# Kernel optimization log

Hardware: AMD Instinct MI355X
Metric: run time of the kernel (lower is better)

Reference implementation:

```python
import jax, jax.numpy as jnp
import numpy as np

VOCAB, EMB, WIN = 32000, 300, 5
H1, H2, NY, NZ = 300, 300, 128, 128
B, S = 32, 512


def setup_inputs() -> dict:
    key = jax.random.key(0)
    ks = jax.random.split(key, 16)
    sc = 0.05
    inp = {
        "x": jax.random.randint(ks[0], (B, S, WIN), 0, VOCAB),
        "emb": jax.random.normal(ks[1], (VOCAB, EMB), jnp.float32) * sc,
        "W_ih1": jax.random.normal(ks[2], (H1, EMB * WIN), jnp.float32) * sc,
        "W_hh1": jax.random.normal(ks[3], (H1, H1), jnp.float32) * sc,
        "b_ih1": jax.random.normal(ks[4], (H1,), jnp.float32) * sc,
        "b_hh1": jax.random.normal(ks[5], (H1,), jnp.float32) * sc,
        "W_ih2": jax.random.normal(ks[6], (H2, H1), jnp.float32) * sc,
        "W_hh2": jax.random.normal(ks[7], (H2, H2), jnp.float32) * sc,
        "b_ih2": jax.random.normal(ks[8], (H2,), jnp.float32) * sc,
        "b_hh2": jax.random.normal(ks[9], (H2,), jnp.float32) * sc,
        "fc1_w": jax.random.normal(ks[10], (NY, H1), jnp.float32) * sc,
        "fc1_b": jax.random.normal(ks[11], (NY,), jnp.float32) * sc,
        "fc2_w": jax.random.normal(ks[12], (NZ, H2), jnp.float32) * sc,
        "fc2_b": jax.random.normal(ks[13], (NZ,), jnp.float32) * sc,
    }
    return inp


def reference(x, emb, W_ih1, W_hh1, b_ih1, b_hh1, W_ih2, W_hh2, b_ih2, b_hh2,
              fc1_w, fc1_b, fc2_w, fc2_b):
    b, s, w = x.shape
    xe = emb[jnp.transpose(x, (1, 0, 2))].reshape(s, b, w * emb.shape[1])
    xe = jax.nn.relu(xe)

    h1_0 = jnp.zeros((b, W_hh1.shape[0]), xe.dtype)
    h2_0 = jnp.zeros((b, W_hh2.shape[0]), xe.dtype)

    def step(carry, xt):
        h1, h2 = carry
        h1 = jnp.tanh(xt @ W_ih1.T + b_ih1 + h1 @ W_hh1.T + b_hh1)
        h2 = jnp.tanh(h1 @ W_ih2.T + b_ih2 + h2 @ W_hh2.T + b_hh2)
        return (h1, h2), (h1, h2)

    _, (out1, out2) = jax.lax.scan(step, (h1_0, h2_0), xe)  # [S,B,H]

    out1 = jnp.transpose(out1, (1, 0, 2)).reshape(b * s, -1)
    out2 = jnp.transpose(out2, (1, 0, 2)).reshape(b * s, -1)
    out1 = out1 @ fc1_w.T + fc1_b
    out2 = out2 @ fc2_w.T + fc2_b
    return (out1, out2)
```

## Files before the change

### kernel.cpp

```cpp
#include <hip/hip_runtime.h>
#include <hip/hip_fp16.h>

#define S_LEN 512
#define BATCH 32
#define CHUNK 16

typedef _Float16 hv2  __attribute__((ext_vector_type(2)));
typedef _Float16 half8 __attribute__((ext_vector_type(8)));
typedef float    f32x4 __attribute__((ext_vector_type(4)));

__device__ __forceinline__ float dot2f(hv2 a, hv2 b, float c) {
#if __has_builtin(__builtin_amdgcn_fdot2)
    return __builtin_amdgcn_fdot2(a, b, c, false);
#else
    return c + (float)a.x * (float)b.x + (float)a.y * (float)b.y;
#endif
}

__device__ __forceinline__ float fast_tanh(float x) {
    float e = __expf(2.f * x);
    return 1.f - 2.f / (e + 1.f);
}

__device__ __forceinline__ void lds_barrier() {
    __asm__ volatile("s_waitcnt lgkmcnt(0)\n\ts_barrier" ::: "memory");
}
__device__ __forceinline__ void vm_drain() {
    __asm__ volatile("s_waitcnt vmcnt(0)" ::: "memory");
}

#define E8   1280000
#define W18  64000
#define W28  12800
#define FF8  5120
#define PREP_TOTAL8 (E8 + W18 + W28 + FF8 + FF8)

__global__ __launch_bounds__(256) void k_prep(
    const float* __restrict__ emb,  const float* __restrict__ Wih1,
    const float* __restrict__ Wih2, const float* __restrict__ fc1w,
    const float* __restrict__ fc2w,
    _Float16* __restrict__ embf, _Float16* __restrict__ Wf1,
    _Float16* __restrict__ Wf2,  _Float16* __restrict__ F1,
    _Float16* __restrict__ F2,   unsigned int* __restrict__ flags)
{
    int gid = blockIdx.x * 256 + threadIdx.x;
    if (gid < 64) flags[gid] = 0u;
    if (gid >= PREP_TOTAL8) return;

    half8 v;
    _Float16* dst;

    if (gid < E8) {
        int row = gid / 40, c8 = (gid - row * 40) * 8;
        #pragma unroll
        for (int j = 0; j < 8; ++j) {
            int c = c8 + j;
            float f = (c < 300) ? emb[(size_t)row * 300 + c] : 0.f;
            v[j] = (_Float16)(f > 0.f ? f : 0.f);
        }
        dst = embf + (size_t)gid * 8;
    } else if (gid < E8 + W18) {
        int i = gid - E8;
        int row = i / 200, c8 = (i - row * 200) * 8;
        #pragma unroll
        for (int j = 0; j < 8; ++j) {
            int c = c8 + j, w = c / 320, cc = c - w * 320;
            float f = (row < 300 && cc < 300) ? Wih1[(size_t)row * 1500 + w * 300 + cc] : 0.f;
            v[j] = (_Float16)f;
        }
        dst = Wf1 + (size_t)i * 8;
    } else if (gid < E8 + W18 + W28) {
        int i = gid - E8 - W18;
        int row = i / 40, c8 = (i - row * 40) * 8;
        #pragma unroll
        for (int j = 0; j < 8; ++j) {
            int c = c8 + j;
            float f = (row < 300 && c < 300) ? Wih2[(size_t)row * 300 + c] : 0.f;
            v[j] = (_Float16)f;
        }
        dst = Wf2 + (size_t)i * 8;
    } else if (gid < E8 + W18 + W28 + FF8) {
        int i = gid - E8 - W18 - W28;
        int row = i / 40, c8 = (i - row * 40) * 8;
        #pragma unroll
        for (int j = 0; j < 8; ++j) {
            int c = c8 + j;
            v[j] = (_Float16)((c < 300) ? fc1w[(size_t)row * 300 + c] : 0.f);
        }
        dst = F1 + (size_t)i * 8;
    } else {
        int i = gid - E8 - W18 - W28 - FF8;
        int row = i / 40, c8 = (i - row * 40) * 8;
        #pragma unroll
        for (int j = 0; j < 8; ++j) {
            int c = c8 + j;
            v[j] = (_Float16)((c < 300) ? fc2w[(size_t)row * 300 + c] : 0.f);
        }
        dst = F2 + (size_t)i * 8;
    }
    *(half8*)dst = v;
}

__global__ __launch_bounds__(256) void k_gemm1_mfma(
    const int* __restrict__ x, const _Float16* __restrict__ embf,
    const _Float16* __restrict__ Wf1, const float* __restrict__ b1,
    const float* __restrict__ b2, float* __restrict__ U)
{
    const int wid  = threadIdx.x >> 6;
    const int lane = threadIdx.x & 63;
    const int m    = lane & 15;
    const int q    = lane >> 4;
    const int r0   = blockIdx.x * 128 + wid * 32;
    const int n0   = blockIdx.y * 160;

    f32x4 acc[2][10];
    #pragma unroll
    for (int i = 0; i < 2; ++i)
        #pragma unroll
        for (int j = 0; j < 10; ++j)
            acc[i][j] = (f32x4){0.f, 0.f, 0.f, 0.f};

    const int rA = r0 + m, rB = r0 + 16 + m;
    const int xbA = ((rA & 31) * S_LEN + (rA >> 5)) * 5;
    const int xbB = ((rB & 31) * S_LEN + (rB >> 5)) * 5;

    for (int w = 0; w < 5; ++w) {
        const int idxA = x[xbA + w];
        const int idxB = x[xbB + w];
        const _Float16* ea = embf + (size_t)idxA * 320;
        const _Float16* eb = embf + (size_t)idxB * 320;
        const _Float16* wb = Wf1 + (size_t)w * 320;
        #pragma unroll
        for (int c = 0; c < 10; ++c) {
            const int k = c * 32 + q * 8;
            half8 a0 = *(const half8*)(ea + k);
            half8 a1 = *(const half8*)(eb + k);
            #pragma unroll
            for (int nt = 0; nt < 10; ++nt) {
                half8 bf = *(const half8*)(wb + (size_t)(n0 + nt * 16 + m) * 1600 + k);
                acc[0][nt] = __builtin_amdgcn_mfma_f32_16x16x32_f16(a0, bf, acc[0][nt], 0, 0, 0);
                acc[1][nt] = __builtin_amdgcn_mfma_f32_16x16x32_f16(a1, bf, acc[1][nt], 0, 0, 0);
            }
        }
    }

    #pragma unroll
    for (int nt = 0; nt < 10; ++nt) {
        const int n = n0 + nt * 16 + m;
        if (n >= 300) continue;
        const float bias = b1[n] + b2[n];
        #pragma unroll
        for (int mt = 0; mt < 2; ++mt) {
            const int rbase = r0 + mt * 16 + q * 4;
            #pragma unroll
            for (int reg = 0; reg < 4; ++reg)
                U[(size_t)(rbase + reg) * 300 + n] = acc[mt][nt][reg] + bias;
        }
    }
}

__global__ __launch_bounds__(256) void k_fc_mfma(
    const _Float16* __restrict__ H1, const _Float16* __restrict__ H2,
    const _Float16* __restrict__ F1, const _Float16* __restrict__ F2,
    const float* __restrict__ fb1, const float* __restrict__ fb2,
    float* __restrict__ out1, float* __restrict__ out2)
{
    const int layer = blockIdx.y;
    const _Float16* H = layer ? H2 : H1;
    const _Float16* F = layer ? F2 : F1;
    const float* bias = layer ? fb2 : fb1;
    float* out        = layer ? out2 : out1;

    const int wid  = threadIdx.x >> 6;
    const int lane = threadIdx.x & 63;
    const int m    = lane & 15;
    const int q    = lane >> 4;
    const int r0   = blockIdx.x * 128 + wid * 32;

    f32x4 acc[2][8];
    #pragma unroll
    for (int i = 0; i < 2; ++i)
        #pragma unroll
        for (int j = 0; j < 8; ++j)
            acc[i][j] = (f32x4){0.f, 0.f, 0.f, 0.f};

    const _Float16* ha = H + (size_t)(r0 + m) * 320;
    const _Float16* hb = H + (size_t)(r0 + 16 + m) * 320;

    #pragma unroll
    for (int c = 0; c < 10; ++c) {
        const int k = c * 32 + q * 8;
        half8 a0 = *(const half8*)(ha + k);
        half8 a1 = *(const half8*)(hb + k);
        #pragma unroll
        for (int nt = 0; nt < 8; ++nt) {
            half8 bf = *(const half8*)(F + (size_t)(nt * 16 + m) * 320 + k);
            acc[0][nt] = __builtin_amdgcn_mfma_f32_16x16x32_f16(a0, bf, acc[0][nt], 0, 0, 0);
            acc[1][nt] = __builtin_amdgcn_mfma_f32_16x16x32_f16(a1, bf, acc[1][nt], 0, 0, 0);
        }
    }

    #pragma unroll
    for (int nt = 0; nt < 8; ++nt) {
        const int n = nt * 16 + m;
        const float bv = bias[n];
        #pragma unroll
        for (int mt = 0; mt < 2; ++mt) {
            #pragma unroll
            for (int reg = 0; reg < 4; ++reg) {
                const int r = r0 + mt * 16 + q * 4 + reg;
                const int oidx = ((r & 31) * S_LEN + (r >> 5)) * 128 + n;
                out[oidx] = acc[mt][nt][reg] + bv;
            }
        }
    }
}

#define LDS_BYTES 60416

__device__ __forceinline__ void load_u_regs(float* up, const float* __restrict__ U1,
                                            int b, int t0) {
    #pragma unroll
    for (int j = 0; j < 10; ++j) {
        int e = threadIdx.x + 512 * j;
        int row = e / 300, col = e - row * 300;
        up[j] = (e < 4800) ? U1[((size_t)((t0 + row) * BATCH + b)) * 300 + col] : 0.f;
    }
}

__global__ __launch_bounds__(512) void k_rec_fused(
    const float* __restrict__ U1, const float* __restrict__ Whh1,
    const _Float16* __restrict__ Wf2, const float* __restrict__ Whh2,
    const float* __restrict__ bih2, const float* __restrict__ bhh2,
    _Float16* __restrict__ H1f, _Float16* __restrict__ H2f,
    unsigned int* __restrict__ flags)
{
    extern __shared__ char smem[];
    float    (*partials)[8][320] = (float(*)[8][320])smem;
    _Float16 (*hc)[320]  = (_Float16(*)[320])(smem + 20480);
    float    (*uc)[304]  = (float(*)[304])(smem + 30720);
    char*     h1sb       = smem + 50176;

    const int tid  = threadIdx.x;
    const int wv   = tid >> 6;
    const int lane = tid & 63;
    const int r    = wv * 40 + lane;
    const bool prod = blockIdx.x < 32;
    const int b    = prod ? (int)blockIdx.x : (int)blockIdx.x - 32;

    for (int i = tid; i < CHUNK * 320; i += 512)
        ((_Float16*)hc)[i] = (_Float16)0.f;

    const float* Whh = prod ? Whh1 : Whh2;
    hv2 wreg[5][20];
    #pragma unroll
    for (int i = 0; i < 5; ++i) {
        const int row = lane + 64 * i;
        const float* wrow = Whh + (size_t)row * 300 + 40 * wv;
        #pragma unroll
        for (int j = 0; j < 20; ++j) {
            const int c0 = 40 * wv + 2 * j;
            hv2 p;
            p.x = (row < 300 && c0     < 300) ? (_Float16)wrow[2 * j]     : (_Float16)0.f;
            p.y = (row < 300 && c0 + 1 < 300) ? (_Float16)wrow[2 * j + 1] : (_Float16)0.f;
            wreg[i][j] = p;
        }
    }

    const float biasc = (!prod && lane < 40 && r < 300) ? (bih2[r] + bhh2[r]) : 0.f;

    unsigned hpk = 0u;

    auto do_step = [&](int s) {
        const int par = s & 1;
        float a0 = 0.f, a1 = 0.f, a2 = 0.f, a3 = 0.f, a4 = 0.f;
        #pragma unroll
        for (int j = 0; j < 20; ++j) {
            const unsigned hj = __builtin_amdgcn_readlane(hpk, j);
            const hv2 hvv = __builtin_bit_cast(hv2, hj);
            a0 = dot2f(wreg[0][j], hvv, a0);
            a1 = dot2f(wreg[1][j], hvv, a1);
            a2 = dot2f(wreg[2][j], hvv, a2);
            a3 = dot2f(wreg[3][j], hvv, a3);
            a4 = dot2f(wreg[4][j], hvv, a4);
        }
        partials[par][wv][lane      ] = a0;
        partials[par][wv][lane +  64] = a1;
        partials[par][wv][lane + 128] = a2;
        partials[par][wv][lane + 192] = a3;
        partials[par][wv][lane + 256] = a4;
        const bool act = (lane < 40) && (r < 300);
        float uval = act ? (uc[s][r] + biasc) : 0.f;
        lds_barrier();
        float v = 0.f;
        if (act) {
            float s01 = partials[par][0][r] + partials[par][1][r];
            float s23 = partials[par][2][r] + partials[par][3][r];
            float s45 = partials[par][4][r] + partials[par][5][r];
            float s67 = partials[par][6][r] + partials[par][7][r];
            v = fast_tanh(uval + ((s01 + s23) + (s45 + s67)));
            hc[s][r] = (_Float16)v;
        }
        const float pa = __shfl(v, 2 * lane);
        const float pb = __shfl(v, 2 * lane + 1);
        hv2 hp2; hp2.x = (_Float16)pa; hp2.y = (_Float16)pb;
        hpk = __builtin_bit_cast(unsigned, hp2);
    };

    if (prod) {
        float upref[10];
        load_u_regs(upref, U1, b, 0);

        for (int c = 0; c < 32; ++c) {
            const int t0 = c * CHUNK;
            if (c > 0) {
                const int tb = t0 - CHUNK;
                for (int i = tid; i < CHUNK * 40; i += 512) {
                    int row = i / 40, c8 = i - row * 40;
                    half8 vv = *(const half8*)&hc[row][c8 * 8];
                    *(half8*)&H1f[((size_t)((tb + row) * BATCH + b)) * 320 + c8 * 8] = vv;
                }
            }
            #pragma unroll
            for (int j = 0; j < 10; ++j) {
                int e = tid + 512 * j;
                if (e < 4800) {
                    int row = e / 300, col = e - row * 300;
                    uc[row][col] = upref[j];
                }
            }
            if (c > 0) {
                vm_drain();
                if (tid == 0)
                    __hip_atomic_store(&flags[b], (unsigned)t0,
                                       __ATOMIC_RELEASE, __HIP_MEMORY_SCOPE_AGENT);
            }
            if (c + 1 < 32)
                load_u_regs(upref, U1, b, t0 + CHUNK);
            lds_barrier();

            for (int s = 0; s < CHUNK; ++s) do_step(s);
            lds_barrier();
        }
        {
            const int tb = S_LEN - CHUNK;
            for (int i = tid; i < CHUNK * 40; i += 512) {
                int row = i / 40, c8 = i - row * 40;
                half8 vv = *(const half8*)&hc[row][c8 * 8];
                *(half8*)&H1f[((size_t)((tb + row) * BATCH + b)) * 320 + c8 * 8] = vv;
            }
            vm_drain();
            if (tid == 0)
                __hip_atomic_store(&flags[b], (unsigned)S_LEN,
                                   __ATOMIC_RELEASE, __HIP_MEMORY_SCOPE_AGENT);
        }
    } else {
        for (int c = 0; c < 32; ++c) {
            const int t0 = c * CHUNK;
            if (c > 0) {
                const int tb = t0 - CHUNK;
                for (int i = tid; i < CHUNK * 40; i += 512) {
                    int row = i / 40, c8 = i - row * 40;
                    half8 vv = *(const half8*)&hc[row][c8 * 8];
                    *(half8*)&H2f[((size_t)((tb + row) * BATCH + b)) * 320 + c8 * 8] = vv;
                }
            }
            if (tid == 0) {
                while (__hip_atomic_load(&flags[b], __ATOMIC_ACQUIRE,
                                         __HIP_MEMORY_SCOPE_AGENT) < (unsigned)(t0 + CHUNK))
                    __builtin_amdgcn_s_sleep(2);
            }
            __syncthreads();

            for (int i = tid; i < CHUNK * 40; i += 512) {
                int row = i / 40, c8 = i - row * 40;
                half8 vv = *(const half8*)&H1f[((size_t)((t0 + row) * BATCH + b)) * 320 + c8 * 8];
                *(half8*)(h1sb + row * 640 + ((c8 * 16) ^ ((row & 7) << 4))) = vv;
            }
            lds_barrier();

            {
                const int lm = lane & 15, lq = lane >> 4;
                for (int nt = wv; nt < 19; nt += 8) {
                    f32x4 acc = (f32x4){0.f, 0.f, 0.f, 0.f};
                    const int n = nt * 16 + lm;
                    const _Float16* wrow2 = Wf2 + (size_t)n * 320;
                    #pragma unroll
                    for (int k0 = 0; k0 < 320; k0 += 32) {
                        half8 av = *(const half8*)(h1sb + lm * 640 +
                                    (((k0 + lq * 8) * 2) ^ ((lm & 7) << 4)));
                        half8 bf = *(const half8*)&wrow2[k0 + lq * 8];
                        acc = __builtin_amdgcn_mfma_f32_16x16x32_f16(av, bf, acc, 0, 0, 0);
                    }
                    #pragma unroll
                    for (int reg = 0; reg < 4; ++reg)
                        uc[lq * 4 + reg][n] = acc[reg];
                }
            }
            lds_barrier();

            for (int s = 0; s < CHUNK; ++s) do_step(s);
            lds_barrier();
        }
        {
            const int tb = S_LEN - CHUNK;
            for (int i = tid; i < CHUNK * 40; i += 512) {
                int row = i / 40, c8 = i - row * 40;
                half8 vv = *(const half8*)&hc[row][c8 * 8];
                *(half8*)&H2f[((size_t)((tb + row) * BATCH + b)) * 320 + c8 * 8] = vv;
            }
        }
    }
}

extern "C" void kernel_launch(void* const* d_in, const int* in_sizes, int n_in,
                              void* d_out, int out_size, void* d_ws, size_t ws_size,
                              hipStream_t stream) {
    const int*   x     = (const int*)d_in[0];
    const float* emb   = (const float*)d_in[1];
    const float* Wih1  = (const float*)d_in[2];
    const float* Whh1  = (const float*)d_in[3];
    const float* bih1  = (const float*)d_in[4];
    const float* bhh1  = (const float*)d_in[5];
    const float* Wih2  = (const float*)d_in[6];
    const float* Whh2  = (const float*)d_in[7];
    const float* bih2  = (const float*)d_in[8];
    const float* bhh2  = (const float*)d_in[9];
    const float* fc1w  = (const float*)d_in[10];
    const float* fc1b  = (const float*)d_in[11];
    const float* fc2w  = (const float*)d_in[12];
    const float* fc2b  = (const float*)d_in[13];

    float* out1 = (float*)d_out;
    float* out2 = out1 + (size_t)16384 * 128;

    char* w = (char*)d_ws;
    float*        U1    = (float*)w;
    _Float16*     H1    = (_Float16*)(w + 19660800);
    _Float16*     Wf1   = (_Float16*)(w + 30146560);
    _Float16*     Wf2   = (_Float16*)(w + 31170560);
    _Float16*     F1    = (_Float16*)(w + 31375360);
    _Float16*     F2    = (_Float16*)(w + 31457280);
    unsigned int* flags = (unsigned int*)(w + 31539200);
    _Float16*     EMBF  = (_Float16*)(w + 31539456);
    _Float16*     H2    = EMBF;

    const int prep_blocks = (PREP_TOTAL8 + 255) / 256;
    k_prep<<<prep_blocks, 256, 0, stream>>>(emb, Wih1, Wih2, fc1w, fc2w,
                                            EMBF, Wf1, Wf2, F1, F2, flags);

    dim3 g(128, 2);
    k_gemm1_mfma<<<g, 256, 0, stream>>>(x, EMBF, Wf1, bih1, bhh1, U1);
    k_rec_fused<<<64, 512, LDS_BYTES, stream>>>(U1, Whh1, Wf2, Whh2, bih2, bhh2,
                                                H1, H2, flags);
    k_fc_mfma<<<g, 256, 0, stream>>>(H1, H2, F1, F2, fc1b, fc2b, out1, out2);
}
```

Before: 902.0 us.

## Fuse both RNN layers into one block per batch with skewed chunk pipeline

Replaces the producer/consumer pair of blocks linked by global flags with a single 512-thread block per batch element. Four waves run layer 1 and four run layer 2 one chunk behind, sharing hidden states through an LDS ring buffer. This removes the global-memory flag handshake and the H1 reload for layer 2. The U1 intermediate is stored as fp16 to halve its traffic. Each wave now holds twice as many recurrent weights in registers (80 columns instead of 40), which raises register pressure. Only 32 blocks run instead of 64, and every step now has two barriers covering both layers.

New measurement: 1.426 ms. 58.1% more time.

```diff
diff --git a/kernel.cpp b/kernel.cpp
--- a/kernel.cpp
+++ b/kernel.cpp
@@ -25,9 +25,6 @@
 __device__ __forceinline__ void lds_barrier() {
     __asm__ volatile("s_waitcnt lgkmcnt(0)\n\ts_barrier" ::: "memory");
 }
-__device__ __forceinline__ void vm_drain() {
-    __asm__ volatile("s_waitcnt vmcnt(0)" ::: "memory");
-}
 
 #define E8   1280000
 #define W18  64000
@@ -41,10 +38,9 @@
     const float* __restrict__ fc2w,
     _Float16* __restrict__ embf, _Float16* __restrict__ Wf1,
     _Float16* __restrict__ Wf2,  _Float16* __restrict__ F1,
-    _Float16* __restrict__ F2,   unsigned int* __restrict__ flags)
+    _Float16* __restrict__ F2)
 {
     int gid = blockIdx.x * 256 + threadIdx.x;
-    if (gid < 64) flags[gid] = 0u;
     if (gid >= PREP_TOTAL8) return;
 
     half8 v;
@@ -104,7 +100,7 @@
 __global__ __launch_bounds__(256) void k_gemm1_mfma(
     const int* __restrict__ x, const _Float16* __restrict__ embf,
     const _Float16* __restrict__ Wf1, const float* __restrict__ b1,
-    const float* __restrict__ b2, float* __restrict__ U)
+    const float* __restrict__ b2, _Float16* __restrict__ U)
 {
     const int wid  = threadIdx.x >> 6;
     const int lane = threadIdx.x & 63;
@@ -154,7 +150,7 @@
             const int rbase = r0 + mt * 16 + q * 4;
             #pragma unroll
             for (int reg = 0; reg < 4; ++reg)
-                U[(size_t)(rbase + reg) * 300 + n] = acc[mt][nt][reg] + bias;
+                U[(size_t)(rbase + reg) * 300 + n] = (_Float16)(acc[mt][nt][reg] + bias);
         }
     }
 }
@@ -216,199 +212,193 @@
     }
 }
 
-#define LDS_BYTES 60416
-
-__device__ __forceinline__ void load_u_regs(float* up, const float* __restrict__ U1,
-                                            int b, int t0) {
-    #pragma unroll
-    for (int j = 0; j < 10; ++j) {
-        int e = threadIdx.x + 512 * j;
-        int row = e / 300, col = e - row * 300;
-        up[j] = (e < 4800) ? U1[((size_t)((t0 + row) * BATCH + b)) * 300 + col] : 0.f;
+#define LDS_BYTES 80256
+
+__device__ __forceinline__ void load_u_pairs(hv2* up, const _Float16* __restrict__ U1h,
+                                             int b, int t0) {
+    #pragma unroll
+    for (int k = 0; k < 5; ++k) {
+        int p = threadIdx.x + 512 * k;
+        if (p < 2400) {
+            int row = p / 150, col2 = (p - row * 150) * 2;
+            up[k] = *(const hv2*)&U1h[((size_t)((t0 + row) * BATCH + b)) * 300 + col2];
+        } else {
+            up[k] = (hv2){(_Float16)0.f, (_Float16)0.f};
+        }
     }
 }
 
 __global__ __launch_bounds__(512) void k_rec_fused(
-    const float* __restrict__ U1, const float* __restrict__ Whh1,
+    const _Float16* __restrict__ U1h, const float* __restrict__ Whh1,
     const _Float16* __restrict__ Wf2, const float* __restrict__ Whh2,
     const float* __restrict__ bih2, const float* __restrict__ bhh2,
-    _Float16* __restrict__ H1f, _Float16* __restrict__ H2f,
-    unsigned int* __restrict__ flags)
+    _Float16* __restrict__ H1f, _Float16* __restrict__ H2f)
 {
     extern __shared__ char smem[];
-    float    (*partials)[8][320] = (float(*)[8][320])smem;
-    _Float16 (*hc)[320]  = (_Float16(*)[320])(smem + 20480);
-    float    (*uc)[304]  = (float(*)[304])(smem + 30720);
-    char*     h1sb       = smem + 50176;
+    float* p1   = (float*)smem;
+    float* p2   = (float*)(smem + 5120);
+    char*  hc1b = smem + 10240;
+    char*  hc2b = smem + 30720;
+    _Float16* uc1h = (_Float16*)(smem + 51200);
+    float (*uc2)[304] = (float(*)[304])(smem + 60800);
 
     const int tid  = threadIdx.x;
-    const int wv   = tid >> 6;
+    const int wid  = tid >> 6;
     const int lane = tid & 63;
-    const int r    = wv * 40 + lane;
-    const bool prod = blockIdx.x < 32;
-    const int b    = prod ? (int)blockIdx.x : (int)blockIdx.x - 32;
-
-    for (int i = tid; i < CHUNK * 320; i += 512)
-        ((_Float16*)hc)[i] = (_Float16)0.f;
-
-    const float* Whh = prod ? Whh1 : Whh2;
-    hv2 wreg[5][20];
-    #pragma unroll
-    for (int i = 0; i < 5; ++i) {
-        const int row = lane + 64 * i;
-        const float* wrow = Whh + (size_t)row * 300 + 40 * wv;
-        #pragma unroll
-        for (int j = 0; j < 20; ++j) {
-            const int c0 = 40 * wv + 2 * j;
-            hv2 p;
-            p.x = (row < 300 && c0     < 300) ? (_Float16)wrow[2 * j]     : (_Float16)0.f;
-            p.y = (row < 300 && c0 + 1 < 300) ? (_Float16)wrow[2 * j + 1] : (_Float16)0.f;
-            wreg[i][j] = p;
-        }
-    }
-
-    const float biasc = (!prod && lane < 40 && r < 300) ? (bih2[r] + bhh2[r]) : 0.f;
-
-    unsigned hpk = 0u;
-
-    auto do_step = [&](int s) {
-        const int par = s & 1;
-        float a0 = 0.f, a1 = 0.f, a2 = 0.f, a3 = 0.f, a4 = 0.f;
-        #pragma unroll
-        for (int j = 0; j < 20; ++j) {
-            const unsigned hj = __builtin_amdgcn_readlane(hpk, j);
-            const hv2 hvv = __builtin_bit_cast(hv2, hj);
-            a0 = dot2f(wreg[0][j], hvv, a0);
-            a1 = dot2f(wreg[1][j], hvv, a1);
-            a2 = dot2f(wreg[2][j], hvv, a2);
-            a3 = dot2f(wreg[3][j], hvv, a3);
-            a4 = dot2f(wreg[4][j], hvv, a4);
-        }
-        partials[par][wv][lane      ] = a0;
-        partials[par][wv][lane +  64] = a1;
-        partials[par][wv][lane + 128] = a2;
-        partials[par][wv][lane + 192] = a3;
-        partials[par][wv][lane + 256] = a4;
-        const bool act = (lane < 40) && (r < 300);
-        float uval = act ? (uc[s][r] + biasc) : 0.f;
+    const int b    = blockIdx.x;
+    const bool isL1 = (wid < 4);
+    const int  ws   = wid & 3;
+    float* pt = isL1 ? p1 : p2;
+
+    for (int i = tid; i < 5120; i += 512)
+        ((half8*)hc1b)[i] = (half8){0,0,0,0,0,0,0,0};
+
+    hv2 wreg[5][40];
+    {
+        const float* W = isL1 ? Whh1 : Whh2;
+        #pragma unroll
+        for (int i = 0; i < 5; ++i) {
+            const int row = lane + 64 * i;
+            const bool rok = row < 300;
+            const float* wr = W + (size_t)row * 300 + 80 * ws;
+            #pragma unroll
+            for (int j = 0; j < 40; ++j) {
+                const int c0 = 80 * ws + 2 * j;
+                hv2 p;
+                p.x = (rok && c0     < 300) ? (_Float16)wr[2 * j]     : (_Float16)0.f;
+                p.y = (rok && c0 + 1 < 300) ? (_Float16)wr[2 * j + 1] : (_Float16)0.f;
+                wreg[i][j] = p;
+            }
+        }
+    }
+
+    const float b2r = (tid < 300) ? (bih2[tid] + bhh2[tid]) : 0.f;
+
+    hv2 upref[5];
+    load_u_pairs(upref, U1h, b, 0);
+
+    for (int c = 0; c <= 32; ++c) {
+        if (c >= 1) {
+            const int tb = (c - 1) * CHUNK;
+            for (int i = tid; i < CHUNK * 40; i += 512) {
+                int rrow = i / 40, c8 = i - rrow * 40;
+                int ring = (tb + rrow) & 31;
+                half8 vv = *(const half8*)(hc1b + ring * 640 +
+                                           ((c8 * 16) ^ ((ring & 7) << 4)));
+                *(half8*)&H1f[((size_t)((tb + rrow) * BATCH + b)) * 320 + c8 * 8] = vv;
+            }
+        }
+        if (c >= 2) {
+            const int tb = (c - 2) * CHUNK;
+            for (int i = tid; i < CHUNK * 40; i += 512) {
+                int rrow = i / 40, c8 = i - rrow * 40;
+                int ring = (tb + rrow) & 31;
+                half8 vv = *(const half8*)(hc2b + ring * 640 +
+                                           ((c8 * 16) ^ ((ring & 7) << 4)));
+                *(half8*)&H2f[((size_t)((tb + rrow) * BATCH + b)) * 320 + c8 * 8] = vv;
+            }
+        }
+
+        if (c < 32) {
+            #pragma unroll
+            for (int k = 0; k < 5; ++k) {
+                int p = tid + 512 * k;
+                if (p < 2400) {
+                    int prow = p / 150, pc2 = (p - prow * 150) * 2;
+                    *(hv2*)&uc1h[(size_t)prow * 300 + pc2] = upref[k];
+                }
+            }
+            if (c + 1 < 32)
+                load_u_pairs(upref, U1h, b, (c + 1) * CHUNK);
+        }
+
+        if (c >= 1) {
+            const int R0 = ((c - 1) * CHUNK) & 31;
+            const int lm = lane & 15, lq = lane >> 4;
+            for (int nt = wid; nt < 19; nt += 8) {
+                f32x4 acc = (f32x4){0.f, 0.f, 0.f, 0.f};
+                const int n = nt * 16 + lm;
+                const _Float16* wrow = Wf2 + (size_t)n * 320;
+                #pragma unroll
+                for (int k0 = 0; k0 < 10; ++k0) {
+                    const int row = R0 + lm;
+                    half8 av = *(const half8*)(hc1b + row * 640 +
+                                 ((k0 * 64 + lq * 16) ^ ((row & 7) << 4)));
+                    half8 bf = *(const half8*)&wrow[k0 * 32 + lq * 8];
+                    acc = __builtin_amdgcn_mfma_f32_16x16x32_f16(av, bf, acc, 0, 0, 0);
+                }
+                #pragma unroll
+                for (int reg = 0; reg < 4; ++reg)
+                    uc2[lq * 4 + reg][n] = acc[reg];
+            }
+        }
         lds_barrier();
-        float v = 0.f;
-        if (act) {
-            float s01 = partials[par][0][r] + partials[par][1][r];
-            float s23 = partials[par][2][r] + partials[par][3][r];
-            float s45 = partials[par][4][r] + partials[par][5][r];
-            float s67 = partials[par][6][r] + partials[par][7][r];
-            v = fast_tanh(uval + ((s01 + s23) + (s45 + s67)));
-            hc[s][r] = (_Float16)v;
-        }
-        const float pa = __shfl(v, 2 * lane);
-        const float pb = __shfl(v, 2 * lane + 1);
-        hv2 hp2; hp2.x = (_Float16)pa; hp2.y = (_Float16)pb;
-        hpk = __builtin_bit_cast(unsigned, hp2);
-    };
-
-    if (prod) {
-        float upref[10];
-        load_u_regs(upref, U1, b, 0);
-
-        for (int c = 0; c < 32; ++c) {
-            const int t0 = c * CHUNK;
-            if (c > 0) {
-                const int tb = t0 - CHUNK;
-                for (int i = tid; i < CHUNK * 40; i += 512) {
-                    int row = i / 40, c8 = i - row * 40;
-                    half8 vv = *(const half8*)&hc[row][c8 * 8];
-                    *(half8*)&H1f[((size_t)((tb + row) * BATCH + b)) * 320 + c8 * 8] = vv;
+
+        #pragma unroll 1
+        for (int s = 0; s < CHUNK; ++s) {
+            float u1v = 0.f, u2v = 0.f;
+            if (tid < 300) {
+                if (c < 32) u1v = (float)uc1h[(size_t)s * 300 + tid];
+                if (c >= 1) u2v = uc2[s][tid] + b2r;
+            }
+            const bool aact = isL1 ? (c < 32) : (c >= 1);
+            if (aact) {
+                const int tm1 = (isL1 ? (c * CHUNK + s) : (c * CHUNK + s - CHUNK)) - 1;
+                const int rr = tm1 & 31;
+                const char* rowp = (isL1 ? hc1b : hc2b) + rr * 640;
+                const int sw = (rr & 7) << 4;
+                float a0 = 0.f, a1 = 0.f, a2 = 0.f, a3 = 0.f, a4 = 0.f;
+                #pragma unroll
+                for (int jj = 0; jj < 10; ++jj) {
+                    half8 q8 = *(const half8*)(rowp + ((ws * 160 + jj * 16) ^ sw));
+                    const hv2* qv = (const hv2*)&q8;
+                    #pragma unroll
+                    for (int j4 = 0; j4 < 4; ++j4) {
+                        const int j = jj * 4 + j4;
+                        a0 = dot2f(wreg[0][j], qv[j4], a0);
+                        a1 = dot2f(wreg[1][j], qv[j4], a1);
+                        a2 = dot2f(wreg[2][j], qv[j4], a2);
+                        a3 = dot2f(wreg[3][j], qv[j4], a3);
+                        a4 = dot2f(wreg[4][j], qv[j4], a4);
+                    }
                 }
-            }
-            #pragma unroll
-            for (int j = 0; j < 10; ++j) {
-                int e = tid + 512 * j;
-                if (e < 4800) {
-                    int row = e / 300, col = e - row * 300;
-                    uc[row][col] = upref[j];
+                pt[ws * 320 + lane      ] = a0;
+                pt[ws * 320 + lane +  64] = a1;
+                pt[ws * 320 + lane + 128] = a2;
+                pt[ws * 320 + lane + 192] = a3;
+                pt[ws * 320 + lane + 256] = a4;
+            }
+            lds_barrier();
+            if (tid < 300) {
+                if (c < 32) {
+                    float sm = (p1[tid] + p1[320 + tid]) +
+                               (p1[640 + tid] + p1[960 + tid]);
+                    float h = fast_tanh(u1v + sm);
+                    const int wr = (c * CHUNK + s) & 31;
+                    *(_Float16*)(hc1b + wr * 640 + ((tid * 2) ^ ((wr & 7) << 4))) =
+                        (_Float16)h;
                 }
-            }
-            if (c > 0) {
-                vm_drain();
-                if (tid == 0)
-                    __hip_atomic_store(&flags[b], (unsigned)t0,
-                                       __ATOMIC_RELEASE, __HIP_MEMORY_SCOPE_AGENT);
-            }
-            if (c + 1 < 32)
-                load_u_regs(upref, U1, b, t0 + CHUNK);
+                if (c >= 1) {
+                    float sm = (p2[tid] + p2[320 + tid]) +
+                               (p2[640 + tid] + p2[960 + tid]);
+                    float h = fast_tanh(u2v + sm);
+                    const int wr = (c * CHUNK + s - CHUNK) & 31;
+                    *(_Float16*)(hc2b + wr * 640 + ((tid * 2) ^ ((wr & 7) << 4))) =
+                        (_Float16)h;
+                }
+            }
             lds_barrier();
-
-            for (int s = 0; s < CHUNK; ++s) do_step(s);
-            lds_barrier();
-        }
-        {
-            const int tb = S_LEN - CHUNK;
-            for (int i = tid; i < CHUNK * 40; i += 512) {
-                int row = i / 40, c8 = i - row * 40;
-                half8 vv = *(const half8*)&hc[row][c8 * 8];
-                *(half8*)&H1f[((size_t)((tb + row) * BATCH + b)) * 320 + c8 * 8] = vv;
-            }
-            vm_drain();
-            if (tid == 0)
-                __hip_atomic_store(&flags[b], (unsigned)S_LEN,
-                                   __ATOMIC_RELEASE, __HIP_MEMORY_SCOPE_AGENT);
-        }
-    } else {
-        for (int c = 0; c < 32; ++c) {
-            const int t0 = c * CHUNK;
-            if (c > 0) {
-                const int tb = t0 - CHUNK;
-                for (int i = tid; i < CHUNK * 40; i += 512) {
-                    int row = i / 40, c8 = i - row * 40;
-                    half8 vv = *(const half8*)&hc[row][c8 * 8];
-                    *(half8*)&H2f[((size_t)((tb + row) * BATCH + b)) * 320 + c8 * 8] = vv;
-                }
-            }
-            if (tid == 0) {
-                while (__hip_atomic_load(&flags[b], __ATOMIC_ACQUIRE,
-                                         __HIP_MEMORY_SCOPE_AGENT) < (unsigned)(t0 + CHUNK))
-                    __builtin_amdgcn_s_sleep(2);
-            }
-            __syncthreads();
-
-            for (int i = tid; i < CHUNK * 40; i += 512) {
-                int row = i / 40, c8 = i - row * 40;
-                half8 vv = *(const half8*)&H1f[((size_t)((t0 + row) * BATCH + b)) * 320 + c8 * 8];
-                *(half8*)(h1sb + row * 640 + ((c8 * 16) ^ ((row & 7) << 4))) = vv;
-            }
-            lds_barrier();
-
-            {
-                const int lm = lane & 15, lq = lane >> 4;
-                for (int nt = wv; nt < 19; nt += 8) {
-                    f32x4 acc = (f32x4){0.f, 0.f, 0.f, 0.f};
-                    const int n = nt * 16 + lm;
-                    const _Float16* wrow2 = Wf2 + (size_t)n * 320;
-                    #pragma unroll
-                    for (int k0 = 0; k0 < 320; k0 += 32) {
-                        half8 av = *(const half8*)(h1sb + lm * 640 +
-                                    (((k0 + lq * 8) * 2) ^ ((lm & 7) << 4)));
-                        half8 bf = *(const half8*)&wrow2[k0 + lq * 8];
-                        acc = __builtin_amdgcn_mfma_f32_16x16x32_f16(av, bf, acc, 0, 0, 0);
-                    }
-                    #pragma unroll
-                    for (int reg = 0; reg < 4; ++reg)
-                        uc[lq * 4 + reg][n] = acc[reg];
-                }
-            }
-            lds_barrier();
-
-            for (int s = 0; s < CHUNK; ++s) do_step(s);
-            lds_barrier();
-        }
-        {
-            const int tb = S_LEN - CHUNK;
-            for (int i = tid; i < CHUNK * 40; i += 512) {
-                int row = i / 40, c8 = i - row * 40;
-                half8 vv = *(const half8*)&hc[row][c8 * 8];
-                *(half8*)&H2f[((size_t)((tb + row) * BATCH + b)) * 320 + c8 * 8] = vv;
-            }
+        }
+    }
+
+    {
+        const int tb = S_LEN - CHUNK;
+        for (int i = tid; i < CHUNK * 40; i += 512) {
+            int rrow = i / 40, c8 = i - rrow * 40;
+            int ring = (tb + rrow) & 31;
+            half8 vv = *(const half8*)(hc2b + ring * 640 +
+                                       ((c8 * 16) ^ ((ring & 7) << 4)));
+            *(half8*)&H2f[((size_t)((tb + rrow) * BATCH + b)) * 320 + c8 * 8] = vv;
         }
     }
 }
@@ -435,23 +425,22 @@
     float* out2 = out1 + (size_t)16384 * 128;
 
     char* w = (char*)d_ws;
-    float*        U1    = (float*)w;
+    _Float16*     U1    = (_Float16*)w;
     _Float16*     H1    = (_Float16*)(w + 19660800);
     _Float16*     Wf1   = (_Float16*)(w + 30146560);
     _Float16*     Wf2   = (_Float16*)(w + 31170560);
     _Float16*     F1    = (_Float16*)(w + 31375360);
     _Float16*     F2    = (_Float16*)(w + 31457280);
-    unsigned int* flags = (unsigned int*)(w + 31539200);
     _Float16*     EMBF  = (_Float16*)(w + 31539456);
     _Float16*     H2    = EMBF;
 
     const int prep_blocks = (PREP_TOTAL8 + 255) / 256;
     k_prep<<<prep_blocks, 256, 0, stream>>>(emb, Wih1, Wih2, fc1w, fc2w,
-                                            EMBF, Wf1, Wf2, F1, F2, flags);
+                                            EMBF, Wf1, Wf2, F1, F2);
 
     dim3 g(128, 2);
     k_gemm1_mfma<<<g, 256, 0, stream>>>(x, EMBF, Wf1, bih1, bhh1, U1);
-    k_rec_fused<<<64, 512, LDS_BYTES, stream>>>(U1, Whh1, Wf2, Whh2, bih2, bhh2,
-                                                H1, H2, flags);
+    k_rec_fused<<<32, 512, LDS_BYTES, stream>>>(U1, Whh1, Wf2, Whh2, bih2, bhh2,
+                                                H1, H2);
     k_fc_mfma<<<g, 256, 0, stream>>>(H1, H2, F1, F2, fc1b, fc2b, out1, out2);
 }
```

## Rewrite recurrence as batched MFMA over 16-batch tiles with separate Wih2 projection blocks

Applied to the files above, without the earlier changes.

Replaces the per-batch recurrence, which used dot2 products, readlane broadcasts and an 8-wave partial-sum reduction in LDS, with an MFMA recurrence. Each of four blocks handles 16 batch columns of one layer, keeping Whh in registers and passing h through double-buffered LDS. Four extra blocks compute the layer-2 input projection in chunks of 16 steps, synchronised with the recurrence blocks through global flags. U1 is now stored in fp16 with padded stride 304, which cuts memory traffic but uses only 8 blocks on the GPU and adds fp16 rounding of the pre-activations.

Result: slower. 1.116 ms (+23.7%).

```diff
diff --git a/kernel.cpp b/kernel.cpp
--- a/kernel.cpp
+++ b/kernel.cpp
@@ -3,19 +3,11 @@
 
 #define S_LEN 512
 #define BATCH 32
-#define CHUNK 16
 
 typedef _Float16 hv2  __attribute__((ext_vector_type(2)));
+typedef _Float16 hv4  __attribute__((ext_vector_type(4)));
 typedef _Float16 half8 __attribute__((ext_vector_type(8)));
 typedef float    f32x4 __attribute__((ext_vector_type(4)));
-
-__device__ __forceinline__ float dot2f(hv2 a, hv2 b, float c) {
-#if __has_builtin(__builtin_amdgcn_fdot2)
-    return __builtin_amdgcn_fdot2(a, b, c, false);
-#else
-    return c + (float)a.x * (float)b.x + (float)a.y * (float)b.y;
-#endif
-}
 
 __device__ __forceinline__ float fast_tanh(float x) {
     float e = __expf(2.f * x);
@@ -104,7 +96,7 @@
 __global__ __launch_bounds__(256) void k_gemm1_mfma(
     const int* __restrict__ x, const _Float16* __restrict__ embf,
     const _Float16* __restrict__ Wf1, const float* __restrict__ b1,
-    const float* __restrict__ b2, float* __restrict__ U)
+    const float* __restrict__ b2, _Float16* __restrict__ U)
 {
     const int wid  = threadIdx.x >> 6;
     const int lane = threadIdx.x & 63;
@@ -147,14 +139,14 @@
     #pragma unroll
     for (int nt = 0; nt < 10; ++nt) {
         const int n = n0 + nt * 16 + m;
-        if (n >= 300) continue;
-        const float bias = b1[n] + b2[n];
+        if (n >= 304) continue;
+        const float bias = (n < 300) ? (b1[n] + b2[n]) : 0.f;
         #pragma unroll
         for (int mt = 0; mt < 2; ++mt) {
             const int rbase = r0 + mt * 16 + q * 4;
             #pragma unroll
             for (int reg = 0; reg < 4; ++reg)
-                U[(size_t)(rbase + reg) * 300 + n] = acc[mt][nt][reg] + bias;
+                U[(size_t)(rbase + reg) * 304 + n] = (_Float16)(acc[mt][nt][reg] + bias);
         }
     }
 }
@@ -170,6 +162,7 @@
     const _Float16* F = layer ? F2 : F1;
     const float* bias = layer ? fb2 : fb1;
     float* out        = layer ? out2 : out1;
+    const int hs      = layer ? 304 : 320;
 
     const int wid  = threadIdx.x >> 6;
     const int lane = threadIdx.x & 63;
@@ -184,8 +177,8 @@
         for (int j = 0; j < 8; ++j)
             acc[i][j] = (f32x4){0.f, 0.f, 0.f, 0.f};
 
-    const _Float16* ha = H + (size_t)(r0 + m) * 320;
-    const _Float16* hb = H + (size_t)(r0 + 16 + m) * 320;
+    const _Float16* ha = H + (size_t)(r0 + m) * hs;
+    const _Float16* hb = H + (size_t)(r0 + 16 + m) * hs;
 
     #pragma unroll
     for (int c = 0; c < 10; ++c) {
@@ -216,199 +209,193 @@
     }
 }
 
-#define LDS_BYTES 60416
-
-__device__ __forceinline__ void load_u_regs(float* up, const float* __restrict__ U1,
-                                            int b, int t0) {
-    #pragma unroll
-    for (int j = 0; j < 10; ++j) {
-        int e = threadIdx.x + 512 * j;
-        int row = e / 300, col = e - row * 300;
-        up[j] = (e < 4800) ? U1[((size_t)((t0 + row) * BATCH + b)) * 300 + col] : 0.f;
-    }
-}
-
-__global__ __launch_bounds__(512) void k_rec_fused(
-    const float* __restrict__ U1, const float* __restrict__ Whh1,
-    const _Float16* __restrict__ Wf2, const float* __restrict__ Whh2,
+#define REC_LDS 20480
+
+__global__ __launch_bounds__(640) void k_rec(
+    const _Float16* __restrict__ U1h, _Float16* __restrict__ U2f,
+    const float* __restrict__ Whh1, const float* __restrict__ Whh2,
+    const _Float16* __restrict__ Wf2,
     const float* __restrict__ bih2, const float* __restrict__ bhh2,
     _Float16* __restrict__ H1f, _Float16* __restrict__ H2f,
     unsigned int* __restrict__ flags)
 {
     extern __shared__ char smem[];
-    float    (*partials)[8][320] = (float(*)[8][320])smem;
-    _Float16 (*hc)[320]  = (_Float16(*)[320])(smem + 20480);
-    float    (*uc)[304]  = (float(*)[304])(smem + 30720);
-    char*     h1sb       = smem + 50176;
-
-    const int tid  = threadIdx.x;
-    const int wv   = tid >> 6;
-    const int lane = tid & 63;
-    const int r    = wv * 40 + lane;
-    const bool prod = blockIdx.x < 32;
-    const int b    = prod ? (int)blockIdx.x : (int)blockIdx.x - 32;
-
-    for (int i = tid; i < CHUNK * 320; i += 512)
-        ((_Float16*)hc)[i] = (_Float16)0.f;
-
-    const float* Whh = prod ? Whh1 : Whh2;
-    hv2 wreg[5][20];
-    #pragma unroll
-    for (int i = 0; i < 5; ++i) {
-        const int row = lane + 64 * i;
-        const float* wrow = Whh + (size_t)row * 300 + 40 * wv;
-        #pragma unroll
-        for (int j = 0; j < 20; ++j) {
-            const int c0 = 40 * wv + 2 * j;
-            hv2 p;
-            p.x = (row < 300 && c0     < 300) ? (_Float16)wrow[2 * j]     : (_Float16)0.f;
-            p.y = (row < 300 && c0 + 1 < 300) ? (_Float16)wrow[2 * j + 1] : (_Float16)0.f;
-            wreg[i][j] = p;
-        }
-    }
-
-    const float biasc = (!prod && lane < 40 && r < 300) ? (bih2[r] + bhh2[r]) : 0.f;
-
-    unsigned hpk = 0u;
-
-    auto do_step = [&](int s) {
-        const int par = s & 1;
-        float a0 = 0.f, a1 = 0.f, a2 = 0.f, a3 = 0.f, a4 = 0.f;
-        #pragma unroll
-        for (int j = 0; j < 20; ++j) {
-            const unsigned hj = __builtin_amdgcn_readlane(hpk, j);
-            const hv2 hvv = __builtin_bit_cast(hv2, hj);
-            a0 = dot2f(wreg[0][j], hvv, a0);
-            a1 = dot2f(wreg[1][j], hvv, a1);
-            a2 = dot2f(wreg[2][j], hvv, a2);
-            a3 = dot2f(wreg[3][j], hvv, a3);
-            a4 = dot2f(wreg[4][j], hvv, a4);
-        }
-        partials[par][wv][lane      ] = a0;
-        partials[par][wv][lane +  64] = a1;
-        partials[par][wv][lane + 128] = a2;
-        partials[par][wv][lane + 192] = a3;
-        partials[par][wv][lane + 256] = a4;
-        const bool act = (lane < 40) && (r < 300);
-        float uval = act ? (uc[s][r] + biasc) : 0.f;
+    const int tid = threadIdx.x;
+    const int wv  = tid >> 6;
+    const int l   = tid & 63;
+    const int m   = l & 15;
+    const int q   = l >> 4;
+    const int bix = blockIdx.x;
+
+    if (bix < 4) {
+        const int layer = bix >> 1;
+        const int nb0   = (bix & 1) * 16;
+        const int batch = nb0 + m;
+        const float* W  = layer ? Whh2 : Whh1;
+        const _Float16* uP = layer ? U2f : U1h;
+        _Float16* hOut  = layer ? H2f : H1f;
+        const int hs    = layer ? 304 : 320;
+
+        half8 aw0[10], aw1[10];
+        {
+            const int rm0 = 32 * wv + m, rm1 = rm0 + 16;
+            #pragma unroll
+            for (int kt = 0; kt < 10; ++kt) {
+                #pragma unroll
+                for (int j = 0; j < 8; ++j) {
+                    const int k = kt * 32 + q * 8 + j;
+                    const bool kok = k < 300;
+                    aw0[kt][j] = (rm0 < 300 && kok) ? (_Float16)W[(size_t)rm0 * 300 + k]
+                                                    : (_Float16)0.f;
+                    aw1[kt][j] = (rm1 < 300 && kok) ? (_Float16)W[(size_t)rm1 * 300 + k]
+                                                    : (_Float16)0.f;
+                }
+            }
+        }
+        const int r0w = 32 * wv + q * 4;
+        const int sw  = (m & 7) << 4;
+        const bool uok1 = (32 * wv + 16) < 304;
+
+        int roff[10];
+        #pragma unroll
+        for (int kt = 0; kt < 10; ++kt)
+            roff[kt] = m * 640 + ((kt * 64 + q * 16) ^ sw);
+        const int woff0 = m * 640 + ((r0w * 2) ^ sw);
+        const int woff1 = m * 640 + (((r0w + 16) * 2) ^ sw);
+
+        half8 z8 = {};
+        ((half8*)smem)[tid] = z8;
         lds_barrier();
-        float v = 0.f;
-        if (act) {
-            float s01 = partials[par][0][r] + partials[par][1][r];
-            float s23 = partials[par][2][r] + partials[par][3][r];
-            float s45 = partials[par][4][r] + partials[par][5][r];
-            float s67 = partials[par][6][r] + partials[par][7][r];
-            v = fast_tanh(uval + ((s01 + s23) + (s45 + s67)));
-            hc[s][r] = (_Float16)v;
-        }
-        const float pa = __shfl(v, 2 * lane);
-        const float pb = __shfl(v, 2 * lane + 1);
-        hv2 hp2; hp2.x = (_Float16)pa; hp2.y = (_Float16)pb;
-        hpk = __builtin_bit_cast(unsigned, hp2);
-    };
-
-    if (prod) {
-        float upref[10];
-        load_u_regs(upref, U1, b, 0);
-
-        for (int c = 0; c < 32; ++c) {
-            const int t0 = c * CHUNK;
-            if (c > 0) {
-                const int tb = t0 - CHUNK;
-                for (int i = tid; i < CHUNK * 40; i += 512) {
-                    int row = i / 40, c8 = i - row * 40;
-                    half8 vv = *(const half8*)&hc[row][c8 * 8];
-                    *(half8*)&H1f[((size_t)((tb + row) * BATCH + b)) * 320 + c8 * 8] = vv;
+
+        hv4 u0 = {}, u1 = {};
+        if (!layer) {
+            u0 = *(const hv4*)&uP[(size_t)batch * 304 + r0w];
+            if (uok1) u1 = *(const hv4*)&uP[(size_t)batch * 304 + r0w + 16];
+        }
+
+        for (int t = 0; t < 512; ++t) {
+            char* rb = smem + (t & 1) * 10240;
+            char* wb = smem + ((t + 1) & 1) * 10240;
+            if (layer && (t & 15) == 0) {
+                if (tid == 0) {
+                    while (__hip_atomic_load(&flags[2 + (t >> 4)], __ATOMIC_ACQUIRE,
+                                             __HIP_MEMORY_SCOPE_AGENT) == 0)
+                        __builtin_amdgcn_s_sleep(8);
                 }
-            }
-            #pragma unroll
-            for (int j = 0; j < 10; ++j) {
-                int e = tid + 512 * j;
-                if (e < 4800) {
-                    int row = e / 300, col = e - row * 300;
-                    uc[row][col] = upref[j];
+                __syncthreads();
+                u0 = *(const hv4*)&uP[(size_t)(t * 32 + batch) * 304 + r0w];
+                if (uok1) u1 = *(const hv4*)&uP[(size_t)(t * 32 + batch) * 304 + r0w + 16];
+            }
+            f32x4 acc0, acc1;
+            #pragma unroll
+            for (int r = 0; r < 4; ++r) {
+                acc0[r] = (float)u0[r];
+                acc1[r] = (float)u1[r];
+            }
+            const int tn = t + 1;
+            if (tn < 512 && (!layer || (tn & 15) != 0)) {
+                u0 = *(const hv4*)&uP[(size_t)(tn * 32 + batch) * 304 + r0w];
+                if (uok1) u1 = *(const hv4*)&uP[(size_t)(tn * 32 + batch) * 304 + r0w + 16];
+            }
+            #pragma unroll
+            for (int kt = 0; kt < 10; ++kt) {
+                half8 bf = *(const half8*)(rb + roff[kt]);
+                acc0 = __builtin_amdgcn_mfma_f32_16x16x32_f16(aw0[kt], bf, acc0, 0, 0, 0);
+                acc1 = __builtin_amdgcn_mfma_f32_16x16x32_f16(aw1[kt], bf, acc1, 0, 0, 0);
+            }
+            hv4 h0, h1;
+            #pragma unroll
+            for (int r = 0; r < 4; ++r) {
+                h0[r] = (_Float16)fast_tanh(acc0[r]);
+                h1[r] = (_Float16)fast_tanh(acc1[r]);
+            }
+            *(hv4*)(wb + woff0) = h0;
+            *(hv4*)(wb + woff1) = h1;
+            _Float16* gp = hOut + (size_t)(t * 32 + batch) * hs + r0w;
+            *(hv4*)gp = h0;
+            if (!layer || uok1) *(hv4*)(gp + 16) = h1;
+
+            if (!layer && (t & 15) == 15) {
+                vm_drain();
+                __syncthreads();
+                if (tid == 0)
+                    __hip_atomic_store(&flags[bix], (unsigned)(t + 1),
+                                       __ATOMIC_RELEASE, __HIP_MEMORY_SCOPE_AGENT);
+            } else {
+                lds_barrier();
+            }
+        }
+    } else {
+        const int nt0 = wv, nt1 = wv + 10;
+        const bool has1 = nt1 < 19;
+
+        half8 wf0[10], wf1[10];
+        #pragma unroll
+        for (int kt = 0; kt < 10; ++kt) {
+            wf0[kt] = *(const half8*)&Wf2[(size_t)(nt0 * 16 + m) * 320 + kt * 32 + q * 8];
+            half8 z = {};
+            wf1[kt] = has1 ? *(const half8*)&Wf2[(size_t)(nt1 * 16 + m) * 320 + kt * 32 + q * 8]
+                           : z;
+        }
+        float bias0[4], bias1[4];
+        #pragma unroll
+        for (int r = 0; r < 4; ++r) {
+            const int n_0 = nt0 * 16 + q * 4 + r;
+            const int n_1 = nt1 * 16 + q * 4 + r;
+            bias0[r] = (n_0 < 300) ? (bih2[n_0] + bhh2[n_0]) : 0.f;
+            bias1[r] = (has1 && n_1 < 300) ? (bih2[n_1] + bhh2[n_1]) : 0.f;
+        }
+
+        for (int c = bix - 4; c < 32; c += 4) {
+            if (tid == 0) {
+                const unsigned need = (unsigned)((c + 1) * 16);
+                while (__hip_atomic_load(&flags[0], __ATOMIC_ACQUIRE,
+                                         __HIP_MEMORY_SCOPE_AGENT) < need ||
+                       __hip_atomic_load(&flags[1], __ATOMIC_ACQUIRE,
+                                         __HIP_MEMORY_SCOPE_AGENT) < need)
+                    __builtin_amdgcn_s_sleep(8);
+            }
+            __syncthreads();
+
+            for (int t = c * 16; t < c * 16 + 16; ++t) {
+                f32x4 a00, a01, a10, a11;
+                #pragma unroll
+                for (int r = 0; r < 4; ++r) {
+                    a00[r] = bias0[r]; a01[r] = bias0[r];
+                    a10[r] = bias1[r]; a11[r] = bias1[r];
                 }
-            }
-            if (c > 0) {
-                vm_drain();
-                if (tid == 0)
-                    __hip_atomic_store(&flags[b], (unsigned)t0,
-                                       __ATOMIC_RELEASE, __HIP_MEMORY_SCOPE_AGENT);
-            }
-            if (c + 1 < 32)
-                load_u_regs(upref, U1, b, t0 + CHUNK);
-            lds_barrier();
-
-            for (int s = 0; s < CHUNK; ++s) do_step(s);
-            lds_barrier();
-        }
-        {
-            const int tb = S_LEN - CHUNK;
-            for (int i = tid; i < CHUNK * 40; i += 512) {
-                int row = i / 40, c8 = i - row * 40;
-                half8 vv = *(const half8*)&hc[row][c8 * 8];
-                *(half8*)&H1f[((size_t)((tb + row) * BATCH + b)) * 320 + c8 * 8] = vv;
+                #pragma unroll
+                for (int kt = 0; kt < 10; ++kt) {
+                    half8 b0 = *(const half8*)&H1f[(size_t)(t * 32 + m) * 320 + kt * 32 + q * 8];
+                    half8 b1 = *(const half8*)&H1f[(size_t)(t * 32 + 16 + m) * 320 + kt * 32 + q * 8];
+                    a00 = __builtin_amdgcn_mfma_f32_16x16x32_f16(wf0[kt], b0, a00, 0, 0, 0);
+                    a01 = __builtin_amdgcn_mfma_f32_16x16x32_f16(wf0[kt], b1, a01, 0, 0, 0);
+                    if (has1) {
+                        a10 = __builtin_amdgcn_mfma_f32_16x16x32_f16(wf1[kt], b0, a10, 0, 0, 0);
+                        a11 = __builtin_amdgcn_mfma_f32_16x16x32_f16(wf1[kt], b1, a11, 0, 0, 0);
+                    }
+                }
+                hv4 s;
+                #pragma unroll
+                for (int r = 0; r < 4; ++r) s[r] = (_Float16)a00[r];
+                *(hv4*)&U2f[(size_t)(t * 32 + m) * 304 + nt0 * 16 + q * 4] = s;
+                #pragma unroll
+                for (int r = 0; r < 4; ++r) s[r] = (_Float16)a01[r];
+                *(hv4*)&U2f[(size_t)(t * 32 + 16 + m) * 304 + nt0 * 16 + q * 4] = s;
+                if (has1) {
+                    #pragma unroll
+                    for (int r = 0; r < 4; ++r) s[r] = (_Float16)a10[r];
+                    *(hv4*)&U2f[(size_t)(t * 32 + m) * 304 + nt1 * 16 + q * 4] = s;
+                    #pragma unroll
+                    for (int r = 0; r < 4; ++r) s[r] = (_Float16)a11[r];
+                    *(hv4*)&U2f[(size_t)(t * 32 + 16 + m) * 304 + nt1 * 16 + q * 4] = s;
+                }
             }
             vm_drain();
+            __syncthreads();
             if (tid == 0)
-                __hip_atomic_store(&flags[b], (unsigned)S_LEN,
+                __hip_atomic_store(&flags[2 + c], 1u,
                                    __ATOMIC_RELEASE, __HIP_MEMORY_SCOPE_AGENT);
-        }
-    } else {
-        for (int c = 0; c < 32; ++c) {
-            const int t0 = c * CHUNK;
-            if (c > 0) {
-                const int tb = t0 - CHUNK;
-                for (int i = tid; i < CHUNK * 40; i += 512) {
-                    int row = i / 40, c8 = i - row * 40;
-                    half8 vv = *(const half8*)&hc[row][c8 * 8];
-                    *(half8*)&H2f[((size_t)((tb + row) * BATCH + b)) * 320 + c8 * 8] = vv;
-                }
-            }
-            if (tid == 0) {
-                while (__hip_atomic_load(&flags[b], __ATOMIC_ACQUIRE,
-                                         __HIP_MEMORY_SCOPE_AGENT) < (unsigned)(t0 + CHUNK))
-                    __builtin_amdgcn_s_sleep(2);
-            }
-            __syncthreads();
-
-            for (int i = tid; i < CHUNK * 40; i += 512) {
-                int row = i / 40, c8 = i - row * 40;
-                half8 vv = *(const half8*)&H1f[((size_t)((t0 + row) * BATCH + b)) * 320 + c8 * 8];
-                *(half8*)(h1sb + row * 640 + ((c8 * 16) ^ ((row & 7) << 4))) = vv;
-            }
-            lds_barrier();
-
-            {
-                const int lm = lane & 15, lq = lane >> 4;
-                for (int nt = wv; nt < 19; nt += 8) {
-                    f32x4 acc = (f32x4){0.f, 0.f, 0.f, 0.f};
-                    const int n = nt * 16 + lm;
-                    const _Float16* wrow2 = Wf2 + (size_t)n * 320;
-                    #pragma unroll
-                    for (int k0 = 0; k0 < 320; k0 += 32) {
-                        half8 av = *(const half8*)(h1sb + lm * 640 +
-                                    (((k0 + lq * 8) * 2) ^ ((lm & 7) << 4)));
-                        half8 bf = *(const half8*)&wrow2[k0 + lq * 8];
-                        acc = __builtin_amdgcn_mfma_f32_16x16x32_f16(av, bf, acc, 0, 0, 0);
-                    }
-                    #pragma unroll
-                    for (int reg = 0; reg < 4; ++reg)
-                        uc[lq * 4 + reg][n] = acc[reg];
-                }
-            }
-            lds_barrier();
-
-            for (int s = 0; s < CHUNK; ++s) do_step(s);
-            lds_barrier();
-        }
-        {
-            const int tb = S_LEN - CHUNK;
-            for (int i = tid; i < CHUNK * 40; i += 512) {
-                int row = i / 40, c8 = i - row * 40;
-                half8 vv = *(const half8*)&hc[row][c8 * 8];
-                *(half8*)&H2f[((size_t)((tb + row) * BATCH + b)) * 320 + c8 * 8] = vv;
-            }
         }
     }
 }
@@ -435,23 +422,24 @@
     float* out2 = out1 + (size_t)16384 * 128;
 
     char* w = (char*)d_ws;
-    float*        U1    = (float*)w;
-    _Float16*     H1    = (_Float16*)(w + 19660800);
-    _Float16*     Wf1   = (_Float16*)(w + 30146560);
-    _Float16*     Wf2   = (_Float16*)(w + 31170560);
-    _Float16*     F1    = (_Float16*)(w + 31375360);
-    _Float16*     F2    = (_Float16*)(w + 31457280);
-    unsigned int* flags = (unsigned int*)(w + 31539200);
-    _Float16*     EMBF  = (_Float16*)(w + 31539456);
-    _Float16*     H2    = EMBF;
+    _Float16*     U1h   = (_Float16*)(w + 0);
+    _Float16*     H1f   = (_Float16*)(w + 9961472);
+    _Float16*     Wf1   = (_Float16*)(w + 20447232);
+    _Float16*     Wf2   = (_Float16*)(w + 21471232);
+    _Float16*     F1    = (_Float16*)(w + 21676032);
+    _Float16*     F2    = (_Float16*)(w + 21757952);
+    unsigned int* flags = (unsigned int*)(w + 21839872);
+    _Float16*     EMBF  = (_Float16*)(w + 21840128);
+    _Float16*     H2f   = EMBF;
+    _Float16*     U2f   = (_Float16*)((char*)EMBF + 9961472);
 
     const int prep_blocks = (PREP_TOTAL8 + 255) / 256;
     k_prep<<<prep_blocks, 256, 0, stream>>>(emb, Wih1, Wih2, fc1w, fc2w,
                                             EMBF, Wf1, Wf2, F1, F2, flags);
 
     dim3 g(128, 2);
-    k_gemm1_mfma<<<g, 256, 0, stream>>>(x, EMBF, Wf1, bih1, bhh1, U1);
-    k_rec_fused<<<64, 512, LDS_BYTES, stream>>>(U1, Whh1, Wf2, Whh2, bih2, bhh2,
-                                                H1, H2, flags);
-    k_fc_mfma<<<g, 256, 0, stream>>>(H1, H2, F1, F2, fc1b, fc2b, out1, out2);
-}
+    k_gemm1_mfma<<<g, 256, 0, stream>>>(x, EMBF, Wf1, bih1, bhh1, U1h);
+    k_rec<<<8, 640, REC_LDS, stream>>>(U1h, U2f, Whh1, Whh2, Wf2,
+                                       bih2, bhh2, H1f, H2f, flags);
+    k_fc_mfma<<<g, 256, 0, stream>>>(H1f, H2f, F1, F2, fc1b, fc2b, out1, out2);
+}
```
